# Kernel tuning notes

Hardware: AMD Instinct MI355X
Metric: run time of the kernel (lower is better)

The kernel has to match this reference:

```python
import jax, jax.numpy as jnp
import numpy as np

N_BONDS = 50000
N_EDGES = 600000
BOND_DIM = 64
SPH_DIM = 64
UNITS = 64


def setup_inputs() -> dict:
    key = jax.random.key(0)
    k1, k2, k3, k4, k5 = jax.random.split(key, 5)
    bond_features = jax.random.normal(k1, (N_BONDS, BOND_DIM), dtype=jnp.float32)
    edges_sph_features = jax.random.normal(k2, (N_EDGES, SPH_DIM), dtype=jnp.float32)
    # column 0: sorted segment ids (tf.math.segment_sum requires sorted ids)
    seg = jnp.sort(jax.random.randint(k3, (N_EDGES,), 0, N_BONDS, dtype=jnp.int32))
    nbr = jax.random.randint(k4, (N_EDGES,), 0, N_BONDS, dtype=jnp.int32)
    edges_neighbor = jnp.stack([seg, nbr], axis=1)  # [n_edges, 2]
    kernel = jax.random.normal(k5, (BOND_DIM + SPH_DIM, UNITS), dtype=jnp.float32) * 0.05
    bias = jnp.zeros((UNITS,), dtype=jnp.float32)
    return {
        "bond_features": bond_features,
        "edges_sph_features": edges_sph_features,
        "edges_neighbor": edges_neighbor,
        "kernel": kernel,
        "bias": bias,
    }


def reference(bond_features, edges_sph_features, edges_neighbor, kernel, bias):
    # gather bond features of the neighboring bond for each edge (line-graph)
    gathered = bond_features[edges_neighbor[:, 1]]            # [E, bond_dim]
    concated = jnp.concatenate([gathered, edges_sph_features], axis=-1)  # [E, bond_dim+sph_dim]
    # scatter-reduce into segments (sorted ids; fixed num_segments for jit)
    aggregated = jax.ops.segment_sum(
        concated, edges_neighbor[:, 0], num_segments=N_BONDS,
        indices_are_sorted=True,
    )  # [n_bonds, bond_dim+sph_dim]
    return aggregated @ kernel + bias
```

## Files before the change

kernel.cpp:

```cpp
#include <hip/hip_runtime.h>

#define N_BONDS 50000
#define N_EDGES 600000
#define R_BONDS 4
#define THREADS 512
#define BONDS_PER_BLOCK 32
#define STARTS_BLOCKS ((N_EDGES + 255) / 256)
#define PREMUL_BLOCKS ((N_BONDS + 31) / 32)

typedef float f4 __attribute__((ext_vector_type(4)));
typedef unsigned short u16x4 __attribute__((ext_vector_type(4)));

__device__ __forceinline__ float bcastf(float v, int l) {
    return __builtin_bit_cast(float, __builtin_amdgcn_readlane(__builtin_bit_cast(int, v), l));
}
__device__ __forceinline__ f4 f4zero() { return (f4){0.f, 0.f, 0.f, 0.f}; }
__device__ __forceinline__ void fma4(f4& a, float s, const f4& b) {
    a.x = fmaf(s, b.x, a.x); a.y = fmaf(s, b.y, a.y);
    a.z = fmaf(s, b.z, a.z); a.w = fmaf(s, b.w, a.w);
}
__device__ __forceinline__ float bf2f(unsigned short u) {
    return __builtin_bit_cast(float, ((unsigned)u) << 16);
}
__device__ __forceinline__ unsigned short f2bf(float f) {
    unsigned u = __builtin_bit_cast(unsigned, f);
    return (unsigned short)((u + 0x7fffu + ((u >> 16) & 1u)) >> 16);
}
__device__ __forceinline__ f4 cvt4(u16x4 u) {
    return (f4){bf2f(u.x), bf2f(u.y), bf2f(u.z), bf2f(u.w)};
}

__global__ __launch_bounds__(256)
void prep(const int* __restrict__ edges, int* __restrict__ starts,
          const float* __restrict__ bond, const float* __restrict__ Kmat,
          unsigned short* __restrict__ bondKb) {
    __shared__ float ldsK[64 * 64];
    const int tid = threadIdx.x;

    if (blockIdx.x < STARTS_BLOCKS) {
        const int e = blockIdx.x * 256 + tid;
        if (e >= N_EDGES) return;
        const int2* edges2 = (const int2*)edges;
        const int s  = edges2[e].x;
        const int sp = (e == 0) ? -1 : edges2[e - 1].x;
        for (int b = sp + 1; b <= s; ++b) starts[b] = e;
        if (e == N_EDGES - 1)
            for (int b = s + 1; b <= N_BONDS; ++b) starts[b] = N_EDGES;
        return;
    }

    const int bid  = blockIdx.x - STARTS_BLOCKS;
    const int lane = tid & 63;
    const int wid  = tid >> 6;
    {
        const f4* K4 = (const f4*)Kmat;
        f4* L4 = (f4*)ldsK;
        #pragma unroll
        for (int i = 0; i < 4; ++i) L4[tid + i * 256] = K4[tid + i * 256];
    }
    __syncthreads();
    const int row0 = bid * 32 + wid * 8;
    if (row0 >= N_BONDS) return;

    float rowv[8], acc[8];
    #pragma unroll
    for (int r = 0; r < 8; ++r) {
        int ri = row0 + r; if (ri >= N_BONDS) ri = N_BONDS - 1;
        rowv[r] = bond[ri * 64 + lane];
        acc[r]  = 0.f;
    }
    #pragma unroll 4
    for (int d = 0; d < 64; ++d) {
        const float k = ldsK[d * 64 + lane];
        #pragma unroll
        for (int r = 0; r < 8; ++r)
            acc[r] = fmaf(bcastf(rowv[r], d), k, acc[r]);
    }
    #pragma unroll
    for (int r = 0; r < 8; ++r)
        if (row0 + r < N_BONDS)
            bondKb[(row0 + r) * 64 + lane] = f2bf(acc[r]);
}

__global__ __launch_bounds__(THREADS, 4)
void fused_gather_segsum_mm(const unsigned short* __restrict__ bondKb,
                            const float* __restrict__ sph,
                            const int*   __restrict__ edges,
                            const float* __restrict__ Kmat,
                            const float* __restrict__ bias,
                            const int*   __restrict__ starts,
                            float* __restrict__ out)
{
    __shared__ float ldsK[64 * 64];
    const int tid  = threadIdx.x;
    const int lane = tid & 63;
    const int wid  = tid >> 6;
    const int fl   = lane & 15;
    const int sg   = lane >> 4;

    {
        const f4* K4 = (const f4*)Kmat;
        f4*       L4 = (f4*)ldsK;
        #pragma unroll
        for (int i = 0; i < 2; ++i) L4[tid + i * THREADS] = K4[1024 + tid + i * THREADS];
    }
    __syncthreads();

    const int b0 = blockIdx.x * BONDS_PER_BLOCK + wid * R_BONDS;
    if (b0 >= N_BONDS) return;

    int st[R_BONDS + 1];
    #pragma unroll
    for (int r = 0; r <= R_BONDS; ++r)
        st[r] = __builtin_amdgcn_readfirstlane(starts[b0 + r]);

    const int eb    = st[0];
    const int total = st[R_BONDS] - eb;

    const u16x4* bk4    = (const u16x4*)bondKb;
    const f4*    sph4   = (const f4*)sph;
    const int2*  edges2 = (const int2*)edges;

    float slotG[R_BONDS], slotS[R_BONDS];
    f4 aG = f4zero(), aS = f4zero();
    int r = 0, cs = 0, bnd = st[1] - eb;

    auto txr = [&](f4 v) -> float {
        v.x += __shfl_xor(v.x, 16); v.y += __shfl_xor(v.y, 16);
        v.z += __shfl_xor(v.z, 16); v.w += __shfl_xor(v.w, 16);
        v.x += __shfl_xor(v.x, 32); v.y += __shfl_xor(v.y, 32);
        v.z += __shfl_xor(v.z, 32); v.w += __shfl_xor(v.w, 32);
        const int src = lane >> 2;
        const float s0 = __shfl(v.x, src), s1 = __shfl(v.y, src);
        const float s2 = __shfl(v.z, src), s3 = __shfl(v.w, src);
        const float r01 = (lane & 1) ? s1 : s0;
        const float r23 = (lane & 1) ? s3 : s2;
        return (lane & 2) ? r23 : r01;
    };

    auto slowpath = [&](int q, f4 GV, f4 SV) {
        const int qe = q + sg;
        while (true) {
            const float m = (qe >= cs && qe < bnd) ? 1.f : 0.f;
            fma4(aG, m, GV); fma4(aS, m, SV);
            if (bnd > q + 4) break;
            const float tG = txr(aG), tS = txr(aS);
            #pragma unroll
            for (int rr = 0; rr < R_BONDS; ++rr)
                if (rr == r) { slotG[rr] = tG; slotS[rr] = tS; }
            aG = f4zero(); aS = f4zero();
            cs = bnd;
            ++r;
            if (r >= R_BONDS) { bnd = 0x7fffffff; break; }
            #pragma unroll
            for (int rr = 2; rr <= R_BONDS; ++rr)
                if (r + 1 == rr) bnd = st[rr] - eb;
        }
    };

    int w0 = 0;
    while (w0 < total) {
        int wlen = total - w0; if (wlen > 64) wlen = 64;
        int2 p = make_int2(0, 0);
        if (lane < wlen) p = edges2[eb + w0 + lane];
        const int ng = (wlen + 3) >> 2;

        u16x4 uA, uB, uC, uD;
        f4 sA, sB, sC, sD;

#define ISS(QQ, UV, SV) do { \
        if ((QQ) < ng) { \
            const int idx_ = (QQ) * 4 + sg; \
            const int nbr_ = __shfl(p.y, idx_); \
            int qe_ = w0 + idx_; if (qe_ >= total) qe_ = total - 1; \
            UV = bk4[nbr_ * 16 + fl]; \
            SV = sph4[(eb + qe_) * 16 + fl]; \
        } else { UV = (u16x4){0,0,0,0}; SV = f4zero(); } } while (0)

#define ACC(QQ, UV, SV) do { \
        const int q_ = w0 + (QQ) * 4; \
        const f4 GVf = cvt4(UV); \
        if (q_ + 4 <= bnd) { aG += GVf; aS += SV; } \
        else slowpath(q_, GVf, SV); } while (0)

        ISS(0, uA, sA); ISS(1, uB, sB); ISS(2, uC, sC); ISS(3, uD, sD);
        int q = 0;
        for (; q + 4 <= ng; q += 4) {
            ACC(q + 0, uA, sA); ISS(q + 4, uA, sA);
            ACC(q + 1, uB, sB); ISS(q + 5, uB, sB);
            ACC(q + 2, uC, sC); ISS(q + 6, uC, sC);
            ACC(q + 3, uD, sD); ISS(q + 7, uD, sD);
        }
        if (q + 0 < ng) ACC(q + 0, uA, sA);
        if (q + 1 < ng) ACC(q + 1, uB, sB);
        if (q + 2 < ng) ACC(q + 2, uC, sC);
#undef ISS
#undef ACC
        w0 += wlen;
    }

    {
        const float tG = txr(aG), tS = txr(aS);
        #pragma unroll
        for (int rr = 0; rr < R_BONDS; ++rr) {
            if (rr == r)     { slotG[rr] = tG;  slotS[rr] = tS; }
            else if (rr > r) { slotG[rr] = 0.f; slotS[rr] = 0.f; }
        }
    }

    float acc[R_BONDS];
    const float bl = bias[lane];
    #pragma unroll
    for (int rr = 0; rr < R_BONDS; ++rr) acc[rr] = slotG[rr] + bl;

    #pragma unroll 4
    for (int d = 0; d < 64; ++d) {
        const float kb = ldsK[d * 64 + lane];
        #pragma unroll
        for (int rr = 0; rr < R_BONDS; ++rr)
            acc[rr] = fmaf(bcastf(slotS[rr], d), kb, acc[rr]);
    }

    #pragma unroll
    for (int rr = 0; rr < R_BONDS; ++rr)
        if (b0 + rr < N_BONDS)
            __builtin_nontemporal_store(acc[rr], &out[(b0 + rr) * 64 + lane]);
}

extern "C" void kernel_launch(void* const* d_in, const int* in_sizes, int n_in,
                              void* d_out, int out_size, void* d_ws, size_t ws_size,
                              hipStream_t stream) {
    const float* bond  = (const float*)d_in[0];
    const float* sph   = (const float*)d_in[1];
    const int*   edges = (const int*)d_in[2];
    const float* Kmat  = (const float*)d_in[3];
    const float* bias  = (const float*)d_in[4];
    float* out = (float*)d_out;

    int*            starts = (int*)d_ws;
    unsigned short* bondKb = (unsigned short*)((char*)d_ws + 262144);

    prep<<<STARTS_BLOCKS + PREMUL_BLOCKS, 256, 0, stream>>>(edges, starts,
                                                            bond, Kmat, bondKb);

    const int nblocks = (N_BONDS + BONDS_PER_BLOCK - 1) / BONDS_PER_BLOCK;
    fused_gather_segsum_mm<<<nblocks, THREADS, 0, stream>>>(bondKb, sph, edges, Kmat,
                                                            bias, starts, out);
}
```

Before: 75.84 us.

## Switch to edge-parallel segment sum with atomics and separate matmul pass

Replaces the bond-parallel fused kernel (which needed a starts/CSR prep pass) with an edge-parallel kernel. In it, each wave handles 64 consecutive edges and flushes segment partial sums with float atomics into zeroed buffers. A third kernel then multiplies the aggregated sph sums by the second half of K and adds the gathered bondK sums plus bias. This removes the starts computation and the per-wave load imbalance, at the cost of two memsets, atomic traffic, an extra round trip through global memory for the 50000x64 intermediates, and more launches.

```diff
diff --git a/kernel.cpp b/kernel.cpp
--- a/kernel.cpp
+++ b/kernel.cpp
@@ -2,11 +2,6 @@
 
 #define N_BONDS 50000
 #define N_EDGES 600000
-#define R_BONDS 4
-#define THREADS 512
-#define BONDS_PER_BLOCK 32
-#define STARTS_BLOCKS ((N_EDGES + 255) / 256)
-#define PREMUL_BLOCKS ((N_BONDS + 31) / 32)
 
 typedef float f4 __attribute__((ext_vector_type(4)));
 typedef unsigned short u16x4 __attribute__((ext_vector_type(4)));
@@ -30,28 +25,11 @@
     return (f4){bf2f(u.x), bf2f(u.y), bf2f(u.z), bf2f(u.w)};
 }
 
-__global__ __launch_bounds__(256)
-void prep(const int* __restrict__ edges, int* __restrict__ starts,
-          const float* __restrict__ bond, const float* __restrict__ Kmat,
-          unsigned short* __restrict__ bondKb) {
+__global__ __launch_bounds__(256, 4)
+void premul_bond(const float* __restrict__ bond, const float* __restrict__ Kmat,
+                 unsigned short* __restrict__ bondKb) {
     __shared__ float ldsK[64 * 64];
-    const int tid = threadIdx.x;
-
-    if (blockIdx.x < STARTS_BLOCKS) {
-        const int e = blockIdx.x * 256 + tid;
-        if (e >= N_EDGES) return;
-        const int2* edges2 = (const int2*)edges;
-        const int s  = edges2[e].x;
-        const int sp = (e == 0) ? -1 : edges2[e - 1].x;
-        for (int b = sp + 1; b <= s; ++b) starts[b] = e;
-        if (e == N_EDGES - 1)
-            for (int b = s + 1; b <= N_BONDS; ++b) starts[b] = N_EDGES;
-        return;
-    }
-
-    const int bid  = blockIdx.x - STARTS_BLOCKS;
-    const int lane = tid & 63;
-    const int wid  = tid >> 6;
+    const int tid = threadIdx.x, lane = tid & 63, wid = tid >> 6;
     {
         const f4* K4 = (const f4*)Kmat;
         f4* L4 = (f4*)ldsK;
@@ -59,7 +37,7 @@
         for (int i = 0; i < 4; ++i) L4[tid + i * 256] = K4[tid + i * 256];
     }
     __syncthreads();
-    const int row0 = bid * 32 + wid * 8;
+    const int row0 = blockIdx.x * 32 + wid * 8;
     if (row0 >= N_BONDS) return;
 
     float rowv[8], acc[8];
@@ -82,149 +60,120 @@
             bondKb[(row0 + r) * 64 + lane] = f2bf(acc[r]);
 }
 
-__global__ __launch_bounds__(THREADS, 4)
-void fused_gather_segsum_mm(const unsigned short* __restrict__ bondKb,
-                            const float* __restrict__ sph,
-                            const int*   __restrict__ edges,
-                            const float* __restrict__ Kmat,
-                            const float* __restrict__ bias,
-                            const int*   __restrict__ starts,
-                            float* __restrict__ out)
+__global__ __launch_bounds__(256, 8)
+void edge_segsum(const unsigned short* __restrict__ bondKb,
+                 const float* __restrict__ sph,
+                 const int*   __restrict__ edges,
+                 float* __restrict__ outG,
+                 float* __restrict__ Sbuf)
 {
-    __shared__ float ldsK[64 * 64];
     const int tid  = threadIdx.x;
     const int lane = tid & 63;
     const int wid  = tid >> 6;
     const int fl   = lane & 15;
     const int sg   = lane >> 4;
 
-    {
-        const f4* K4 = (const f4*)Kmat;
-        f4*       L4 = (f4*)ldsK;
-        #pragma unroll
-        for (int i = 0; i < 2; ++i) L4[tid + i * THREADS] = K4[1024 + tid + i * THREADS];
-    }
-    __syncthreads();
-
-    const int b0 = blockIdx.x * BONDS_PER_BLOCK + wid * R_BONDS;
-    if (b0 >= N_BONDS) return;
-
-    int st[R_BONDS + 1];
-    #pragma unroll
-    for (int r = 0; r <= R_BONDS; ++r)
-        st[r] = __builtin_amdgcn_readfirstlane(starts[b0 + r]);
-
-    const int eb    = st[0];
-    const int total = st[R_BONDS] - eb;
-
-    const u16x4* bk4    = (const u16x4*)bondKb;
-    const f4*    sph4   = (const f4*)sph;
-    const int2*  edges2 = (const int2*)edges;
-
-    float slotG[R_BONDS], slotS[R_BONDS];
+    const int W  = blockIdx.x * 4 + wid;
+    const int e0 = W * 64;
+    if (e0 >= N_EDGES) return;
+
+    const int2 p = ((const int2*)edges)[e0 + lane];
+    const u16x4* bk4 = (const u16x4*)bondKb;
+    const f4*    s4  = (const f4*)sph;
+
     f4 aG = f4zero(), aS = f4zero();
-    int r = 0, cs = 0, bnd = st[1] - eb;
-
-    auto txr = [&](f4 v) -> float {
+    int cur = __builtin_amdgcn_readlane(p.x, 0);
+
+    auto closeseg = [&](int s) {
+        f4 g = aG, v = aS;
+        g.x += __shfl_xor(g.x, 16); g.y += __shfl_xor(g.y, 16);
+        g.z += __shfl_xor(g.z, 16); g.w += __shfl_xor(g.w, 16);
+        g.x += __shfl_xor(g.x, 32); g.y += __shfl_xor(g.y, 32);
+        g.z += __shfl_xor(g.z, 32); g.w += __shfl_xor(g.w, 32);
         v.x += __shfl_xor(v.x, 16); v.y += __shfl_xor(v.y, 16);
         v.z += __shfl_xor(v.z, 16); v.w += __shfl_xor(v.w, 16);
         v.x += __shfl_xor(v.x, 32); v.y += __shfl_xor(v.y, 32);
         v.z += __shfl_xor(v.z, 32); v.w += __shfl_xor(v.w, 32);
-        const int src = lane >> 2;
-        const float s0 = __shfl(v.x, src), s1 = __shfl(v.y, src);
-        const float s2 = __shfl(v.z, src), s3 = __shfl(v.w, src);
-        const float r01 = (lane & 1) ? s1 : s0;
-        const float r23 = (lane & 1) ? s3 : s2;
-        return (lane & 2) ? r23 : r01;
+        if (sg == 0) {
+            float* og = &outG[s * 64 + fl * 4];
+            unsafeAtomicAdd(og + 0, g.x); unsafeAtomicAdd(og + 1, g.y);
+            unsafeAtomicAdd(og + 2, g.z); unsafeAtomicAdd(og + 3, g.w);
+            float* os = &Sbuf[s * 64 + fl * 4];
+            unsafeAtomicAdd(os + 0, v.x); unsafeAtomicAdd(os + 1, v.y);
+            unsafeAtomicAdd(os + 2, v.z); unsafeAtomicAdd(os + 3, v.w);
+        }
+        aG = f4zero(); aS = f4zero();
     };
 
-    auto slowpath = [&](int q, f4 GV, f4 SV) {
-        const int qe = q + sg;
-        while (true) {
-            const float m = (qe >= cs && qe < bnd) ? 1.f : 0.f;
-            fma4(aG, m, GV); fma4(aS, m, SV);
-            if (bnd > q + 4) break;
-            const float tG = txr(aG), tS = txr(aS);
+    auto accq = [&](int q, u16x4 uv, f4 sv) {
+        const f4 gv = cvt4(uv);
+        const int sA = __builtin_amdgcn_readlane(p.x, 4 * q);
+        const int sD = __builtin_amdgcn_readlane(p.x, 4 * q + 3);
+        if (sA == cur && sD == cur) {
+            aG += gv; aS += sv;
+        } else {
             #pragma unroll
-            for (int rr = 0; rr < R_BONDS; ++rr)
-                if (rr == r) { slotG[rr] = tG; slotS[rr] = tS; }
-            aG = f4zero(); aS = f4zero();
-            cs = bnd;
-            ++r;
-            if (r >= R_BONDS) { bnd = 0x7fffffff; break; }
-            #pragma unroll
-            for (int rr = 2; rr <= R_BONDS; ++rr)
-                if (r + 1 == rr) bnd = st[rr] - eb;
+            for (int j = 0; j < 4; ++j) {
+                const int se = __builtin_amdgcn_readlane(p.x, 4 * q + j);
+                if (se != cur) { closeseg(cur); cur = se; }
+                const float m = (sg == j) ? 1.f : 0.f;
+                fma4(aG, m, gv); fma4(aS, m, sv);
+            }
         }
     };
 
-    int w0 = 0;
-    while (w0 < total) {
-        int wlen = total - w0; if (wlen > 64) wlen = 64;
-        int2 p = make_int2(0, 0);
-        if (lane < wlen) p = edges2[eb + w0 + lane];
-        const int ng = (wlen + 3) >> 2;
-
-        u16x4 uA, uB, uC, uD;
-        f4 sA, sB, sC, sD;
-
-#define ISS(QQ, UV, SV) do { \
-        if ((QQ) < ng) { \
-            const int idx_ = (QQ) * 4 + sg; \
-            const int nbr_ = __shfl(p.y, idx_); \
-            int qe_ = w0 + idx_; if (qe_ >= total) qe_ = total - 1; \
-            UV = bk4[nbr_ * 16 + fl]; \
-            SV = sph4[(eb + qe_) * 16 + fl]; \
-        } else { UV = (u16x4){0,0,0,0}; SV = f4zero(); } } while (0)
-
-#define ACC(QQ, UV, SV) do { \
-        const int q_ = w0 + (QQ) * 4; \
-        const f4 GVf = cvt4(UV); \
-        if (q_ + 4 <= bnd) { aG += GVf; aS += SV; } \
-        else slowpath(q_, GVf, SV); } while (0)
-
-        ISS(0, uA, sA); ISS(1, uB, sB); ISS(2, uC, sC); ISS(3, uD, sD);
-        int q = 0;
-        for (; q + 4 <= ng; q += 4) {
-            ACC(q + 0, uA, sA); ISS(q + 4, uA, sA);
-            ACC(q + 1, uB, sB); ISS(q + 5, uB, sB);
-            ACC(q + 2, uC, sC); ISS(q + 6, uC, sC);
-            ACC(q + 3, uD, sD); ISS(q + 7, uD, sD);
-        }
-        if (q + 0 < ng) ACC(q + 0, uA, sA);
-        if (q + 1 < ng) ACC(q + 1, uB, sB);
-        if (q + 2 < ng) ACC(q + 2, uC, sC);
-#undef ISS
-#undef ACC
-        w0 += wlen;
-    }
-
+    auto iss = [&](int q, u16x4& uv, f4& sv) {
+        const int nbr = __shfl(p.y, 4 * q + sg);
+        uv = bk4[nbr * 16 + fl];
+        sv = s4[(e0 + 4 * q + sg) * 16 + fl];
+    };
+
+    u16x4 uA, uB; f4 vA, vB;
+    iss(0, uA, vA); iss(1, uB, vB);
+    #pragma unroll
+    for (int q = 0; q < 16; q += 2) {
+        if (q + 2 < 16) { accq(q, uA, vA); iss(q + 2, uA, vA); }
+        else              accq(q, uA, vA);
+        if (q + 3 < 16) { accq(q + 1, uB, vB); iss(q + 3, uB, vB); }
+        else              accq(q + 1, uB, vB);
+    }
+    closeseg(cur);
+}
+
+__global__ __launch_bounds__(256, 4)
+void finish_mm(const float* __restrict__ Sbuf, const float* __restrict__ Kmat,
+               const float* __restrict__ bias, float* __restrict__ out) {
+    __shared__ float ldsK[64 * 64];
+    const int tid = threadIdx.x, lane = tid & 63, wid = tid >> 6;
     {
-        const float tG = txr(aG), tS = txr(aS);
-        #pragma unroll
-        for (int rr = 0; rr < R_BONDS; ++rr) {
-            if (rr == r)     { slotG[rr] = tG;  slotS[rr] = tS; }
-            else if (rr > r) { slotG[rr] = 0.f; slotS[rr] = 0.f; }
-        }
-    }
-
-    float acc[R_BONDS];
+        const f4* K4 = (const f4*)Kmat;
+        f4* L4 = (f4*)ldsK;
+        #pragma unroll
+        for (int i = 0; i < 4; ++i) L4[tid + i * 256] = K4[1024 + tid + i * 256];
+    }
+    __syncthreads();
+    const int row0 = blockIdx.x * 32 + wid * 8;
+    if (row0 >= N_BONDS) return;
+
     const float bl = bias[lane];
-    #pragma unroll
-    for (int rr = 0; rr < R_BONDS; ++rr) acc[rr] = slotG[rr] + bl;
-
+    float rowv[8], acc[8];
+    #pragma unroll
+    for (int r = 0; r < 8; ++r) {
+        int ri = row0 + r; if (ri >= N_BONDS) ri = N_BONDS - 1;
+        rowv[r] = Sbuf[ri * 64 + lane];
+        acc[r]  = out[ri * 64 + lane] + bl;
+    }
     #pragma unroll 4
     for (int d = 0; d < 64; ++d) {
-        const float kb = ldsK[d * 64 + lane];
-        #pragma unroll
-        for (int rr = 0; rr < R_BONDS; ++rr)
-            acc[rr] = fmaf(bcastf(slotS[rr], d), kb, acc[rr]);
-    }
-
-    #pragma unroll
-    for (int rr = 0; rr < R_BONDS; ++rr)
-        if (b0 + rr < N_BONDS)
-            __builtin_nontemporal_store(acc[rr], &out[(b0 + rr) * 64 + lane]);
+        const float k = ldsK[d * 64 + lane];
+        #pragma unroll
+        for (int r = 0; r < 8; ++r)
+            acc[r] = fmaf(bcastf(rowv[r], d), k, acc[r]);
+    }
+    #pragma unroll
+    for (int r = 0; r < 8; ++r)
+        if (row0 + r < N_BONDS)
+            __builtin_nontemporal_store(acc[r], &out[(row0 + r) * 64 + lane]);
 }
 
 extern "C" void kernel_launch(void* const* d_in, const int* in_sizes, int n_in,
@@ -237,13 +186,18 @@
     const float* bias  = (const float*)d_in[4];
     float* out = (float*)d_out;
 
-    int*            starts = (int*)d_ws;
-    unsigned short* bondKb = (unsigned short*)((char*)d_ws + 262144);
-
-    prep<<<STARTS_BLOCKS + PREMUL_BLOCKS, 256, 0, stream>>>(edges, starts,
-                                                            bond, Kmat, bondKb);
-
-    const int nblocks = (N_BONDS + BONDS_PER_BLOCK - 1) / BONDS_PER_BLOCK;
-    fused_gather_segsum_mm<<<nblocks, THREADS, 0, stream>>>(bondKb, sph, edges, Kmat,
-                                                            bias, starts, out);
-}
+    const size_t rowBytes = (size_t)N_BONDS * 64 * sizeof(float);
+    float*          Sbuf   = (float*)d_ws;
+    unsigned short* bondKb = (unsigned short*)((char*)d_ws + rowBytes);
+
+    hipMemsetAsync(out,  0, rowBytes, stream);
+    hipMemsetAsync(Sbuf, 0, rowBytes, stream);
+
+    premul_bond<<<(N_BONDS + 31) / 32, 256, 0, stream>>>(bond, Kmat, bondKb);
+
+    const int nwaves  = N_EDGES / 64;
+    const int nblocks = (nwaves + 3) / 4;
+    edge_segsum<<<nblocks, 256, 0, stream>>>(bondKb, sph, edges, out, Sbuf);
+
+    finish_mm<<<(N_BONDS + 31) / 32, 256, 0, stream>>>(Sbuf, Kmat, bias, out);
+}
```

Result: slower. 173.9 us (+129.3%).

## Split gather and sph streaming into separate blocks, add finishing matmul kernel

Applied to the files above, without the earlier changes.

The fused kernel is split into a segment-sum kernel in which even blocks gather the premultiplied bf16 bond rows and odd blocks stream the sph rows. Each block writes its partial result to the output or to a scratch buffer. A third kernel then multiplies the summed sph rows by the lower half of K, adds bias and the gathered part, and writes the output. The goal is to separate the latency-bound random gather from the bandwidth-bound streaming and raise occupancy with more bonds per wave. The cost is an extra 12.8MB buffer round trip, a read-modify-write of the output and one more kernel launch.

```diff
diff --git a/kernel.cpp b/kernel.cpp
--- a/kernel.cpp
+++ b/kernel.cpp
@@ -2,11 +2,12 @@
 
 #define N_BONDS 50000
 #define N_EDGES 600000
-#define R_BONDS 4
-#define THREADS 512
+#define R_BONDS 8
+#define THREADS 256
 #define BONDS_PER_BLOCK 32
 #define STARTS_BLOCKS ((N_EDGES + 255) / 256)
 #define PREMUL_BLOCKS ((N_BONDS + 31) / 32)
+#define MAIN_BBLKS ((N_BONDS + BONDS_PER_BLOCK - 1) / BONDS_PER_BLOCK)
 
 typedef float f4 __attribute__((ext_vector_type(4)));
 typedef unsigned short u16x4 __attribute__((ext_vector_type(4)));
@@ -82,31 +83,22 @@
             bondKb[(row0 + r) * 64 + lane] = f2bf(acc[r]);
 }
 
-__global__ __launch_bounds__(THREADS, 4)
-void fused_gather_segsum_mm(const unsigned short* __restrict__ bondKb,
-                            const float* __restrict__ sph,
-                            const int*   __restrict__ edges,
-                            const float* __restrict__ Kmat,
-                            const float* __restrict__ bias,
-                            const int*   __restrict__ starts,
-                            float* __restrict__ out)
+__global__ __launch_bounds__(THREADS, 8)
+void split_segsum(const unsigned short* __restrict__ bondKb,
+                  const float* __restrict__ sph,
+                  const int*   __restrict__ edges,
+                  const int*   __restrict__ starts,
+                  float* __restrict__ outG,
+                  float* __restrict__ Sbuf)
 {
-    __shared__ float ldsK[64 * 64];
     const int tid  = threadIdx.x;
     const int lane = tid & 63;
     const int wid  = tid >> 6;
     const int fl   = lane & 15;
     const int sg   = lane >> 4;
-
-    {
-        const f4* K4 = (const f4*)Kmat;
-        f4*       L4 = (f4*)ldsK;
-        #pragma unroll
-        for (int i = 0; i < 2; ++i) L4[tid + i * THREADS] = K4[1024 + tid + i * THREADS];
-    }
-    __syncthreads();
-
-    const int b0 = blockIdx.x * BONDS_PER_BLOCK + wid * R_BONDS;
+    const bool isStream = (blockIdx.x & 1);
+
+    const int b0 = (blockIdx.x >> 1) * BONDS_PER_BLOCK + wid * R_BONDS;
     if (b0 >= N_BONDS) return;
 
     int st[R_BONDS + 1];
@@ -117,12 +109,8 @@
     const int eb    = st[0];
     const int total = st[R_BONDS] - eb;
 
-    const u16x4* bk4    = (const u16x4*)bondKb;
-    const f4*    sph4   = (const f4*)sph;
-    const int2*  edges2 = (const int2*)edges;
-
-    float slotG[R_BONDS], slotS[R_BONDS];
-    f4 aG = f4zero(), aS = f4zero();
+    float slot[R_BONDS];
+    f4 aX = f4zero();
     int r = 0, cs = 0, bnd = st[1] - eb;
 
     auto txr = [&](f4 v) -> float {
@@ -138,17 +126,17 @@
         return (lane & 2) ? r23 : r01;
     };
 
-    auto slowpath = [&](int q, f4 GV, f4 SV) {
+    auto slowpath = [&](int q, f4 XV) {
         const int qe = q + sg;
         while (true) {
             const float m = (qe >= cs && qe < bnd) ? 1.f : 0.f;
-            fma4(aG, m, GV); fma4(aS, m, SV);
+            fma4(aX, m, XV);
             if (bnd > q + 4) break;
-            const float tG = txr(aG), tS = txr(aS);
+            const float tX = txr(aX);
             #pragma unroll
             for (int rr = 0; rr < R_BONDS; ++rr)
-                if (rr == r) { slotG[rr] = tG; slotS[rr] = tS; }
-            aG = f4zero(); aS = f4zero();
+                if (rr == r) slot[rr] = tX;
+            aX = f4zero();
             cs = bnd;
             ++r;
             if (r >= R_BONDS) { bnd = 0x7fffffff; break; }
@@ -157,74 +145,121 @@
                 if (r + 1 == rr) bnd = st[rr] - eb;
         }
     };
-
-    int w0 = 0;
-    while (w0 < total) {
-        int wlen = total - w0; if (wlen > 64) wlen = 64;
-        int2 p = make_int2(0, 0);
-        if (lane < wlen) p = edges2[eb + w0 + lane];
-        const int ng = (wlen + 3) >> 2;
-
-        u16x4 uA, uB, uC, uD;
-        f4 sA, sB, sC, sD;
-
-#define ISS(QQ, UV, SV) do { \
-        if ((QQ) < ng) { \
-            const int idx_ = (QQ) * 4 + sg; \
-            const int nbr_ = __shfl(p.y, idx_); \
-            int qe_ = w0 + idx_; if (qe_ >= total) qe_ = total - 1; \
-            UV = bk4[nbr_ * 16 + fl]; \
-            SV = sph4[(eb + qe_) * 16 + fl]; \
-        } else { UV = (u16x4){0,0,0,0}; SV = f4zero(); } } while (0)
-
-#define ACC(QQ, UV, SV) do { \
-        const int q_ = w0 + (QQ) * 4; \
-        const f4 GVf = cvt4(UV); \
-        if (q_ + 4 <= bnd) { aG += GVf; aS += SV; } \
-        else slowpath(q_, GVf, SV); } while (0)
-
-        ISS(0, uA, sA); ISS(1, uB, sB); ISS(2, uC, sC); ISS(3, uD, sD);
+    auto accq = [&](int q_, f4 XV) {
+        if (q_ + 4 <= bnd) aX += XV;
+        else slowpath(q_, XV);
+    };
+
+    if (!isStream) {
+        const u16x4* bk4    = (const u16x4*)bondKb;
+        const int2*  edges2 = (const int2*)edges;
+        int w0 = 0;
+        while (w0 < total) {
+            int wlen = total - w0; if (wlen > 64) wlen = 64;
+            int2 p = make_int2(0, 0);
+            if (lane < wlen) p = edges2[eb + w0 + lane];
+            const int ng = (wlen + 3) >> 2;
+            u16x4 uA, uB, uC, uD;
+
+#define ISSG(QQ, UV) do { \
+            if ((QQ) < ng) { \
+                const int nbr_ = __shfl(p.y, (QQ) * 4 + sg); \
+                UV = bk4[nbr_ * 16 + fl]; \
+            } else UV = (u16x4){0,0,0,0}; } while (0)
+#define ACCG(QQ, UV) accq(w0 + (QQ) * 4, cvt4(UV))
+
+            ISSG(0, uA); ISSG(1, uB); ISSG(2, uC); ISSG(3, uD);
+            int q = 0;
+            for (; q + 4 <= ng; q += 4) {
+                ACCG(q + 0, uA); ISSG(q + 4, uA);
+                ACCG(q + 1, uB); ISSG(q + 5, uB);
+                ACCG(q + 2, uC); ISSG(q + 6, uC);
+                ACCG(q + 3, uD); ISSG(q + 7, uD);
+            }
+            if (q + 0 < ng) ACCG(q + 0, uA);
+            if (q + 1 < ng) ACCG(q + 1, uB);
+            if (q + 2 < ng) ACCG(q + 2, uC);
+#undef ISSG
+#undef ACCG
+            w0 += wlen;
+        }
+    } else {
+        const f4* s4 = (const f4*)sph;
+        const int nq = (total + 3) >> 2;
+        f4 vA, vB, vC, vD;
+
+#define ISSS(QQ, SV) do { \
+        if ((QQ) < nq) { \
+            int qe_ = (QQ) * 4 + sg; if (qe_ >= total) qe_ = total - 1; \
+            SV = s4[(eb + qe_) * 16 + fl]; \
+        } else SV = f4zero(); } while (0)
+#define ACCS(QQ, SV) accq((QQ) * 4, SV)
+
+        ISSS(0, vA); ISSS(1, vB); ISSS(2, vC); ISSS(3, vD);
         int q = 0;
-        for (; q + 4 <= ng; q += 4) {
-            ACC(q + 0, uA, sA); ISS(q + 4, uA, sA);
-            ACC(q + 1, uB, sB); ISS(q + 5, uB, sB);
-            ACC(q + 2, uC, sC); ISS(q + 6, uC, sC);
-            ACC(q + 3, uD, sD); ISS(q + 7, uD, sD);
-        }
-        if (q + 0 < ng) ACC(q + 0, uA, sA);
-        if (q + 1 < ng) ACC(q + 1, uB, sB);
-        if (q + 2 < ng) ACC(q + 2, uC, sC);
-#undef ISS
-#undef ACC
-        w0 += wlen;
+        for (; q + 4 <= nq; q += 4) {
+            ACCS(q + 0, vA); ISSS(q + 4, vA);
+            ACCS(q + 1, vB); ISSS(q + 5, vB);
+            ACCS(q + 2, vC); ISSS(q + 6, vC);
+            ACCS(q + 3, vD); ISSS(q + 7, vD);
+        }
+        if (q + 0 < nq) ACCS(q + 0, vA);
+        if (q + 1 < nq) ACCS(q + 1, vB);
+        if (q + 2 < nq) ACCS(q + 2, vC);
+#undef ISSS
+#undef ACCS
     }
 
     {
-        const float tG = txr(aG), tS = txr(aS);
+        const float tX = txr(aX);
         #pragma unroll
         for (int rr = 0; rr < R_BONDS; ++rr) {
-            if (rr == r)     { slotG[rr] = tG;  slotS[rr] = tS; }
-            else if (rr > r) { slotG[rr] = 0.f; slotS[rr] = 0.f; }
-        }
-    }
-
-    float acc[R_BONDS];
+            if (rr == r)     slot[rr] = tX;
+            else if (rr > r) slot[rr] = 0.f;
+        }
+    }
+
+    float* dst = isStream ? Sbuf : outG;
+    #pragma unroll
+    for (int rr = 0; rr < R_BONDS; ++rr)
+        if (b0 + rr < N_BONDS)
+            __builtin_nontemporal_store(slot[rr], &dst[(b0 + rr) * 64 + lane]);
+}
+
+__global__ __launch_bounds__(256, 4)
+void finish_mm(const float* __restrict__ Sbuf, const float* __restrict__ Kmat,
+               const float* __restrict__ bias, float* __restrict__ out) {
+    __shared__ float ldsK[64 * 64];
+    const int tid = threadIdx.x, lane = tid & 63, wid = tid >> 6;
+    {
+        const f4* K4 = (const f4*)Kmat;
+        f4* L4 = (f4*)ldsK;
+        #pragma unroll
+        for (int i = 0; i < 4; ++i) L4[tid + i * 256] = K4[1024 + tid + i * 256];
+    }
+    __syncthreads();
+    const int row0 = blockIdx.x * 32 + wid * 8;
+    if (row0 >= N_BONDS) return;
+
     const float bl = bias[lane];
-    #pragma unroll
-    for (int rr = 0; rr < R_BONDS; ++rr) acc[rr] = slotG[rr] + bl;
-
+    float rowv[8], acc[8];
+    #pragma unroll
+    for (int r = 0; r < 8; ++r) {
+        int ri = row0 + r; if (ri >= N_BONDS) ri = N_BONDS - 1;
+        rowv[r] = Sbuf[ri * 64 + lane];
+        acc[r]  = out[ri * 64 + lane] + bl;
+    }
     #pragma unroll 4
     for (int d = 0; d < 64; ++d) {
-        const float kb = ldsK[d * 64 + lane];
-        #pragma unroll
-        for (int rr = 0; rr < R_BONDS; ++rr)
-            acc[rr] = fmaf(bcastf(slotS[rr], d), kb, acc[rr]);
-    }
-
-    #pragma unroll
-    for (int rr = 0; rr < R_BONDS; ++rr)
-        if (b0 + rr < N_BONDS)
-            __builtin_nontemporal_store(acc[rr], &out[(b0 + rr) * 64 + lane]);
+        const float k = ldsK[d * 64 + lane];
+        #pragma unroll
+        for (int r = 0; r < 8; ++r)
+            acc[r] = fmaf(bcastf(rowv[r], d), k, acc[r]);
+    }
+    #pragma unroll
+    for (int r = 0; r < 8; ++r)
+        if (row0 + r < N_BONDS)
+            __builtin_nontemporal_store(acc[r], &out[(row0 + r) * 64 + lane]);
 }
 
 extern "C" void kernel_launch(void* const* d_in, const int* in_sizes, int n_in,
@@ -237,13 +272,16 @@
     const float* bias  = (const float*)d_in[4];
     float* out = (float*)d_out;
 
+    const size_t rowBytes = (size_t)N_BONDS * 64 * sizeof(float);
     int*            starts = (int*)d_ws;
-    unsigned short* bondKb = (unsigned short*)((char*)d_ws + 262144);
+    float*          Sbuf   = (float*)((char*)d_ws + 262144);
+    unsigned short* bondKb = (unsigned short*)((char*)d_ws + 262144 + rowBytes);
 
     prep<<<STARTS_BLOCKS + PREMUL_BLOCKS, 256, 0, stream>>>(edges, starts,
                                                             bond, Kmat, bondKb);
 
-    const int nblocks = (N_BONDS + BONDS_PER_BLOCK - 1) / BONDS_PER_BLOCK;
-    fused_gather_segsum_mm<<<nblocks, THREADS, 0, stream>>>(bondKb, sph, edges, Kmat,
-                                                            bias, starts, out);
-}
+    split_segsum<<<2 * MAIN_BBLKS, THREADS, 0, stream>>>(bondKb, sph, edges,
+                                                         starts, out, Sbuf);
+
+    finish_mm<<<PREMUL_BLOCKS, 256, 0, stream>>>(Sbuf, Kmat, bias, out);
+}
```

Result: slower. 88.93 us (+17.3%).

## Split fused kernel into separate gather-segsum and streaming sph-segsum-matmul kernels

Applied to the files above, without the earlier changes.

The single fused kernel is split in two. The first gathers the premultiplied bf16 bond rows by neighbor index and segment-sums them into an fp32 workspace. The second streams the sph features, segment-sums them, multiplies by the lower half of K, and adds the gathered partial sums. Each wave now handles 8 bonds in 256-thread blocks, and the index loads are software-pipelined. The intent is to separate the random-access gather from the sequential stream so each kernel can get better occupancy and memory-level parallelism, at the cost of an extra launch and a 12.8MB intermediate round-trip.

```diff
diff --git a/kernel.cpp b/kernel.cpp
--- a/kernel.cpp
+++ b/kernel.cpp
@@ -2,11 +2,11 @@
 
 #define N_BONDS 50000
 #define N_EDGES 600000
-#define R_BONDS 4
-#define THREADS 512
+#define R_BONDS 8
 #define BONDS_PER_BLOCK 32
 #define STARTS_BLOCKS ((N_EDGES + 255) / 256)
 #define PREMUL_BLOCKS ((N_BONDS + 31) / 32)
+#define MAIN_BLOCKS ((N_BONDS + BONDS_PER_BLOCK - 1) / BONDS_PER_BLOCK)
 
 typedef float f4 __attribute__((ext_vector_type(4)));
 typedef unsigned short u16x4 __attribute__((ext_vector_type(4)));
@@ -82,47 +82,35 @@
             bondKb[(row0 + r) * 64 + lane] = f2bf(acc[r]);
 }
 
-__global__ __launch_bounds__(THREADS, 4)
-void fused_gather_segsum_mm(const unsigned short* __restrict__ bondKb,
-                            const float* __restrict__ sph,
-                            const int*   __restrict__ edges,
-                            const float* __restrict__ Kmat,
-                            const float* __restrict__ bias,
-                            const int*   __restrict__ starts,
-                            float* __restrict__ out)
+__global__ __launch_bounds__(256, 8)
+void gather_segsum(const unsigned short* __restrict__ bondKb,
+                   const int* __restrict__ edges,
+                   const int* __restrict__ starts,
+                   float* __restrict__ Gsum)
 {
-    __shared__ float ldsK[64 * 64];
     const int tid  = threadIdx.x;
     const int lane = tid & 63;
     const int wid  = tid >> 6;
     const int fl   = lane & 15;
     const int sg   = lane >> 4;
 
-    {
-        const f4* K4 = (const f4*)Kmat;
-        f4*       L4 = (f4*)ldsK;
-        #pragma unroll
-        for (int i = 0; i < 2; ++i) L4[tid + i * THREADS] = K4[1024 + tid + i * THREADS];
-    }
-    __syncthreads();
-
     const int b0 = blockIdx.x * BONDS_PER_BLOCK + wid * R_BONDS;
     if (b0 >= N_BONDS) return;
 
     int st[R_BONDS + 1];
     #pragma unroll
-    for (int r = 0; r <= R_BONDS; ++r)
-        st[r] = __builtin_amdgcn_readfirstlane(starts[b0 + r]);
-
+    for (int r = 0; r <= R_BONDS; ++r) {
+        int ix = b0 + r; if (ix > N_BONDS) ix = N_BONDS;
+        st[r] = __builtin_amdgcn_readfirstlane(starts[ix]);
+    }
     const int eb    = st[0];
     const int total = st[R_BONDS] - eb;
-
-    const u16x4* bk4    = (const u16x4*)bondKb;
-    const f4*    sph4   = (const f4*)sph;
-    const int2*  edges2 = (const int2*)edges;
-
-    float slotG[R_BONDS], slotS[R_BONDS];
-    f4 aG = f4zero(), aS = f4zero();
+    const int nq    = (total + 3) >> 2;
+
+    const u16x4* bk4 = (const u16x4*)bondKb;
+
+    float slot[R_BONDS];
+    f4 aX = f4zero();
     int r = 0, cs = 0, bnd = st[1] - eb;
 
     auto txr = [&](f4 v) -> float {
@@ -137,81 +125,179 @@
         const float r23 = (lane & 1) ? s3 : s2;
         return (lane & 2) ? r23 : r01;
     };
-
-    auto slowpath = [&](int q, f4 GV, f4 SV) {
+    auto slowpath = [&](int q, f4 XV) {
         const int qe = q + sg;
         while (true) {
             const float m = (qe >= cs && qe < bnd) ? 1.f : 0.f;
-            fma4(aG, m, GV); fma4(aS, m, SV);
+            fma4(aX, m, XV);
             if (bnd > q + 4) break;
-            const float tG = txr(aG), tS = txr(aS);
+            const float tX = txr(aX);
             #pragma unroll
-            for (int rr = 0; rr < R_BONDS; ++rr)
-                if (rr == r) { slotG[rr] = tG; slotS[rr] = tS; }
-            aG = f4zero(); aS = f4zero();
+            for (int rr = 0; rr < R_BONDS; ++rr) if (rr == r) slot[rr] = tX;
+            aX = f4zero();
             cs = bnd;
             ++r;
             if (r >= R_BONDS) { bnd = 0x7fffffff; break; }
             #pragma unroll
-            for (int rr = 2; rr <= R_BONDS; ++rr)
-                if (r + 1 == rr) bnd = st[rr] - eb;
-        }
-    };
-
-    int w0 = 0;
-    while (w0 < total) {
-        int wlen = total - w0; if (wlen > 64) wlen = 64;
-        int2 p = make_int2(0, 0);
-        if (lane < wlen) p = edges2[eb + w0 + lane];
-        const int ng = (wlen + 3) >> 2;
-
-        u16x4 uA, uB, uC, uD;
-        f4 sA, sB, sC, sD;
-
-#define ISS(QQ, UV, SV) do { \
-        if ((QQ) < ng) { \
-            const int idx_ = (QQ) * 4 + sg; \
-            const int nbr_ = __shfl(p.y, idx_); \
-            int qe_ = w0 + idx_; if (qe_ >= total) qe_ = total - 1; \
-            UV = bk4[nbr_ * 16 + fl]; \
-            SV = sph4[(eb + qe_) * 16 + fl]; \
-        } else { UV = (u16x4){0,0,0,0}; SV = f4zero(); } } while (0)
-
-#define ACC(QQ, UV, SV) do { \
-        const int q_ = w0 + (QQ) * 4; \
-        const f4 GVf = cvt4(UV); \
-        if (q_ + 4 <= bnd) { aG += GVf; aS += SV; } \
-        else slowpath(q_, GVf, SV); } while (0)
-
-        ISS(0, uA, sA); ISS(1, uB, sB); ISS(2, uC, sC); ISS(3, uD, sD);
-        int q = 0;
-        for (; q + 4 <= ng; q += 4) {
-            ACC(q + 0, uA, sA); ISS(q + 4, uA, sA);
-            ACC(q + 1, uB, sB); ISS(q + 5, uB, sB);
-            ACC(q + 2, uC, sC); ISS(q + 6, uC, sC);
-            ACC(q + 3, uD, sD); ISS(q + 7, uD, sD);
-        }
-        if (q + 0 < ng) ACC(q + 0, uA, sA);
-        if (q + 1 < ng) ACC(q + 1, uB, sB);
-        if (q + 2 < ng) ACC(q + 2, uC, sC);
-#undef ISS
-#undef ACC
-        w0 += wlen;
+            for (int rr = 2; rr <= R_BONDS; ++rr) if (r + 1 == rr) bnd = st[rr] - eb;
+        }
+    };
+    auto accX = [&](int Q, f4 XV) {
+        const int q_ = Q * 4;
+        if (q_ + 4 <= bnd) aX += XV;
+        else slowpath(q_, XV);
+    };
+    auto loadIdx = [&](int Q) -> int {
+        if (Q >= nq) return 0;
+        int e = 4 * Q + sg;
+        e = (e < total) ? e : total - 1;
+        return edges[2 * (eb + e) + 1];
+    };
+
+    if (nq > 0) {
+        int ia0 = loadIdx(0), ia1 = loadIdx(1), ia2 = loadIdx(2), ia3 = loadIdx(3);
+        int ib0 = loadIdx(4), ib1 = loadIdx(5), ib2 = loadIdx(6), ib3 = loadIdx(7);
+        for (int Q = 0; Q < nq; Q += 4) {
+            u16x4 x0 = bk4[ia0 * 16 + fl];
+            u16x4 x1 = (Q + 1 < nq) ? bk4[ia1 * 16 + fl] : (u16x4){0,0,0,0};
+            u16x4 x2 = (Q + 2 < nq) ? bk4[ia2 * 16 + fl] : (u16x4){0,0,0,0};
+            u16x4 x3 = (Q + 3 < nq) ? bk4[ia3 * 16 + fl] : (u16x4){0,0,0,0};
+            ia0 = ib0; ia1 = ib1; ia2 = ib2; ia3 = ib3;
+            ib0 = loadIdx(Q + 8);  ib1 = loadIdx(Q + 9);
+            ib2 = loadIdx(Q + 10); ib3 = loadIdx(Q + 11);
+            accX(Q + 0, cvt4(x0));
+            if (Q + 1 < nq) accX(Q + 1, cvt4(x1));
+            if (Q + 2 < nq) accX(Q + 2, cvt4(x2));
+            if (Q + 3 < nq) accX(Q + 3, cvt4(x3));
+        }
     }
 
     {
-        const float tG = txr(aG), tS = txr(aS);
+        const float tX = txr(aX);
         #pragma unroll
         for (int rr = 0; rr < R_BONDS; ++rr) {
-            if (rr == r)     { slotG[rr] = tG;  slotS[rr] = tS; }
-            else if (rr > r) { slotG[rr] = 0.f; slotS[rr] = 0.f; }
-        }
+            if (rr == r)     slot[rr] = tX;
+            else if (rr > r) slot[rr] = 0.f;
+        }
+    }
+    #pragma unroll
+    for (int rr = 0; rr < R_BONDS; ++rr)
+        if (b0 + rr < N_BONDS)
+            __builtin_nontemporal_store(slot[rr], &Gsum[(b0 + rr) * 64 + lane]);
+}
+
+__global__ __launch_bounds__(256, 6)
+void stream_segsum_mm(const float* __restrict__ sph,
+                      const float* __restrict__ Kmat,
+                      const float* __restrict__ bias,
+                      const int* __restrict__ starts,
+                      const float* __restrict__ Gsum,
+                      float* __restrict__ out)
+{
+    __shared__ float ldsK[64 * 64];
+    const int tid  = threadIdx.x;
+    const int lane = tid & 63;
+    const int wid  = tid >> 6;
+    const int fl   = lane & 15;
+    const int sg   = lane >> 4;
+
+    {
+        const f4* K4 = (const f4*)Kmat;
+        f4* L4 = (f4*)ldsK;
+        #pragma unroll
+        for (int i = 0; i < 4; ++i) L4[tid + i * 256] = K4[1024 + tid + i * 256];
+    }
+    __syncthreads();
+
+    const int b0 = blockIdx.x * BONDS_PER_BLOCK + wid * R_BONDS;
+    if (b0 >= N_BONDS) return;
+
+    int st[R_BONDS + 1];
+    #pragma unroll
+    for (int r = 0; r <= R_BONDS; ++r) {
+        int ix = b0 + r; if (ix > N_BONDS) ix = N_BONDS;
+        st[r] = __builtin_amdgcn_readfirstlane(starts[ix]);
+    }
+    const int eb    = st[0];
+    const int total = st[R_BONDS] - eb;
+    const int nq    = (total + 3) >> 2;
+
+    const f4* sph4 = (const f4*)sph;
+
+    float slotS[R_BONDS];
+    f4 aX = f4zero();
+    int r = 0, cs = 0, bnd = st[1] - eb;
+
+    auto txr = [&](f4 v) -> float {
+        v.x += __shfl_xor(v.x, 16); v.y += __shfl_xor(v.y, 16);
+        v.z += __shfl_xor(v.z, 16); v.w += __shfl_xor(v.w, 16);
+        v.x += __shfl_xor(v.x, 32); v.y += __shfl_xor(v.y, 32);
+        v.z += __shfl_xor(v.z, 32); v.w += __shfl_xor(v.w, 32);
+        const int src = lane >> 2;
+        const float s0 = __shfl(v.x, src), s1 = __shfl(v.y, src);
+        const float s2 = __shfl(v.z, src), s3 = __shfl(v.w, src);
+        const float r01 = (lane & 1) ? s1 : s0;
+        const float r23 = (lane & 1) ? s3 : s2;
+        return (lane & 2) ? r23 : r01;
+    };
+    auto slowpath = [&](int q, f4 XV) {
+        const int qe = q + sg;
+        while (true) {
+            const float m = (qe >= cs && qe < bnd) ? 1.f : 0.f;
+            fma4(aX, m, XV);
+            if (bnd > q + 4) break;
+            const float tX = txr(aX);
+            #pragma unroll
+            for (int rr = 0; rr < R_BONDS; ++rr) if (rr == r) slotS[rr] = tX;
+            aX = f4zero();
+            cs = bnd;
+            ++r;
+            if (r >= R_BONDS) { bnd = 0x7fffffff; break; }
+            #pragma unroll
+            for (int rr = 2; rr <= R_BONDS; ++rr) if (r + 1 == rr) bnd = st[rr] - eb;
+        }
+    };
+    auto accX = [&](int Q, f4 XV) {
+        const int q_ = Q * 4;
+        if (q_ + 4 <= bnd) aX += XV;
+        else slowpath(q_, XV);
+    };
+
+    for (int Q = 0; Q < nq; Q += 4) {
+        int e0 = 4 * Q + sg;       e0 = (e0 < total) ? e0 : total - 1;
+        int e1 = 4 * (Q + 1) + sg; e1 = (e1 < total) ? e1 : total - 1;
+        int e2 = 4 * (Q + 2) + sg; e2 = (e2 < total) ? e2 : total - 1;
+        int e3 = 4 * (Q + 3) + sg; e3 = (e3 < total) ? e3 : total - 1;
+        f4 x0 = sph4[(eb + e0) * 16 + fl];
+        f4 x1 = (Q + 1 < nq) ? sph4[(eb + e1) * 16 + fl] : f4zero();
+        f4 x2 = (Q + 2 < nq) ? sph4[(eb + e2) * 16 + fl] : f4zero();
+        f4 x3 = (Q + 3 < nq) ? sph4[(eb + e3) * 16 + fl] : f4zero();
+        accX(Q + 0, x0);
+        if (Q + 1 < nq) accX(Q + 1, x1);
+        if (Q + 2 < nq) accX(Q + 2, x2);
+        if (Q + 3 < nq) accX(Q + 3, x3);
+    }
+
+    {
+        const float tX = txr(aX);
+        #pragma unroll
+        for (int rr = 0; rr < R_BONDS; ++rr) {
+            if (rr == r)     slotS[rr] = tX;
+            else if (rr > r) slotS[rr] = 0.f;
+        }
+    }
+
+    float gv[R_BONDS];
+    #pragma unroll
+    for (int rr = 0; rr < R_BONDS; ++rr) {
+        int ri = b0 + rr; if (ri >= N_BONDS) ri = N_BONDS - 1;
+        gv[rr] = Gsum[ri * 64 + lane];
     }
 
     float acc[R_BONDS];
     const float bl = bias[lane];
     #pragma unroll
-    for (int rr = 0; rr < R_BONDS; ++rr) acc[rr] = slotG[rr] + bl;
+    for (int rr = 0; rr < R_BONDS; ++rr) acc[rr] = bl;
 
     #pragma unroll 4
     for (int d = 0; d < 64; ++d) {
@@ -224,7 +310,7 @@
     #pragma unroll
     for (int rr = 0; rr < R_BONDS; ++rr)
         if (b0 + rr < N_BONDS)
-            __builtin_nontemporal_store(acc[rr], &out[(b0 + rr) * 64 + lane]);
+            __builtin_nontemporal_store(acc[rr] + gv[rr], &out[(b0 + rr) * 64 + lane]);
 }
 
 extern "C" void kernel_launch(void* const* d_in, const int* in_sizes, int n_in,
@@ -237,13 +323,14 @@
     const float* bias  = (const float*)d_in[4];
     float* out = (float*)d_out;
 
+    const size_t rowBytes = (size_t)N_BONDS * 64 * sizeof(float);
     int*            starts = (int*)d_ws;
-    unsigned short* bondKb = (unsigned short*)((char*)d_ws + 262144);
+    float*          Gsum   = (float*)((char*)d_ws + 262144);
+    unsigned short* bondKb = (unsigned short*)((char*)d_ws + 262144 + rowBytes);
 
     prep<<<STARTS_BLOCKS + PREMUL_BLOCKS, 256, 0, stream>>>(edges, starts,
                                                             bond, Kmat, bondKb);
-
-    const int nblocks = (N_BONDS + BONDS_PER_BLOCK - 1) / BONDS_PER_BLOCK;
-    fused_gather_segsum_mm<<<nblocks, THREADS, 0, stream>>>(bondKb, sph, edges, Kmat,
-                                                            bias, starts, out);
-}
+    gather_segsum<<<MAIN_BLOCKS, 256, 0, stream>>>(bondKb, edges, starts, Gsum);
+    stream_segsum_mm<<<MAIN_BLOCKS, 256, 0, stream>>>(sph, Kmat, bias, starts,
+                                                      Gsum, out);
+}
```

Measured after the change: 88.34 us. +16.5%, slower.
